# Kernel optimization log

Hardware: AMD Instinct MI355X
Metric: run time of the kernel (lower is better)

Reference implementation:

```python
import jax, jax.numpy as jnp
import numpy as np

EPS_IN = 1e-5   # InstanceNorm2d default eps
EPS_VAR = 1e-6  # clamp on attention variance

def instance_norm(x):
    # x: (b, c, h, w); affine=False, biased variance over spatial dims
    mean = jnp.mean(x, axis=(2, 3), keepdims=True)
    var = jnp.var(x, axis=(2, 3), keepdims=True)
    return (x - mean) * jax.lax.rsqrt(var + EPS_IN)

def setup_inputs() -> dict:
    key = jax.random.key(0)
    k1, k2, k3, k4 = jax.random.split(key, 4)
    shp = (4, 512, 64, 64)
    return {
        "c_x": jax.random.normal(k1, shp, dtype=jnp.float32),
        "s_x": jax.random.normal(k2, shp, dtype=jnp.float32),
        "c_1x": jax.random.normal(k3, shp, dtype=jnp.float32),
        "s_1x": jax.random.normal(k4, shp, dtype=jnp.float32),
    }

def reference(c_x, s_x, c_1x, s_1x):
    b, v_dim, h, w = c_x.shape
    hw = h * w
    # Q: (b, hw, qk), K: (b, qk, hw), V: (b, hw, v)
    Q = instance_norm(c_1x).reshape(b, -1, hw).transpose(0, 2, 1)
    K = instance_norm(s_1x).reshape(b, -1, s_1x.shape[2] * s_1x.shape[3])
    V = s_x.reshape(b, v_dim, -1).transpose(0, 2, 1)
    # attention over spatial tokens
    A = jax.nn.softmax(jnp.einsum('bqc,bck->bqk', Q, K), axis=-1)
    M = jnp.einsum('bqk,bkv->bqv', A, V)              # weighted mean
    Var = jnp.einsum('bqk,bkv->bqv', A, V * V) - M * M  # weighted variance
    S = jnp.sqrt(jnp.clip(Var, EPS_VAR, None))
    # back to (b, v, h, w)
    M = M.reshape(b, h, w, -1).transpose(0, 3, 1, 2)
    S = S.reshape(b, h, w, -1).transpose(0, 3, 1, 2)
    return S * instance_norm(c_x) + M
```

## Files before the change

### kernel.cpp

```cpp
#include <hip/hip_runtime.h>
#include <cmath>


#define B_  4
#define C_  512
#define HW_ 4096

typedef _Float16 f16;
typedef _Float16 f16x8 __attribute__((ext_vector_type(8)));
typedef float    f32x4 __attribute__((ext_vector_type(4)));

__device__ __forceinline__ f32x4 mfma16(f16x8 a, f16x8 b, f32x4 c) {
  return __builtin_amdgcn_mfma_f32_16x16x32_f16(a, b, c, 0, 0, 0);
}
__device__ __forceinline__ void g2l16(const f16* g, f16* l) {
  __builtin_amdgcn_global_load_lds(
      (const __attribute__((address_space(1))) void*)g,
      (__attribute__((address_space(3))) void*)l, 16, 0, 0);
}

__global__ __launch_bounds__(256) void k_stats(
    const float* __restrict__ cx, const float* __restrict__ c1,
    const float* __restrict__ s1,
    float2* __restrict__ cxs, float2* __restrict__ c1s, float2* __restrict__ s1s) {
  int c = blockIdx.x, b = blockIdx.y, t = blockIdx.z;
  const float* src = (t == 0 ? cx : (t == 1 ? c1 : s1)) + (size_t)(b * C_ + c) * HW_;
  float s = 0.f, q = 0.f;
  const float4* src4 = (const float4*)src;
  for (int i = threadIdx.x; i < HW_ / 4; i += 256) {
    float4 v = src4[i];
    s += v.x + v.y + v.z + v.w;
    q += v.x * v.x + v.y * v.y + v.z * v.z + v.w * v.w;
  }
#pragma unroll
  for (int off = 1; off < 64; off <<= 1) {
    s += __shfl_xor(s, off);
    q += __shfl_xor(q, off);
  }
  __shared__ float ss[4], sq[4];
  int wv = threadIdx.x >> 6;
  if ((threadIdx.x & 63) == 0) { ss[wv] = s; sq[wv] = q; }
  __syncthreads();
  if (threadIdx.x == 0) {
    float S = ss[0] + ss[1] + ss[2] + ss[3];
    float Q = sq[0] + sq[1] + sq[2] + sq[3];
    float mean = S * (1.f / HW_);
    float var = Q * (1.f / HW_) - mean * mean;
    float2 r;
    r.x = mean;
    r.y = rsqrtf(var + 1e-5f);
    (t == 0 ? cxs : (t == 1 ? c1s : s1s))[b * C_ + c] = r;
  }
}

__global__ __launch_bounds__(256) void k_prept(
    const float* __restrict__ src, const float2* __restrict__ st,
    f16* __restrict__ dst) {
  int pb = blockIdx.x * 64, cb = blockIdx.y * 64, b = blockIdx.z;
  __shared__ float t[64][65];
  int tj = threadIdx.x & 63, tr = threadIdx.x >> 6;
#pragma unroll 4
  for (int p = 0; p < 16; ++p) {
    int cl = p * 4 + tr;
    float2 mr = st[b * C_ + cb + cl];
    float v = src[(size_t)(b * C_ + cb + cl) * HW_ + pb + tj];
    t[cl][tj] = (v - mr.x) * mr.y;
  }
  __syncthreads();
#pragma unroll 4
  for (int p = 0; p < 16; ++p) {
    int pr = p * 4 + tr;
    dst[(size_t)(b * HW_ + pb + pr) * C_ + cb + tj] = (f16)t[tj][pr];
  }
}

__global__ __launch_bounds__(256) void k_prepv(const float* __restrict__ src,
                                               f16* __restrict__ dst) {
  int gid = blockIdx.x * 256 + threadIdx.x;
  const float4* s = (const float4*)src + (size_t)gid * 2;
  float4 v0 = s[0], v1 = s[1];
  f16x8 v = {(f16)v0.x, (f16)v0.y, (f16)v0.z, (f16)v0.w,
             (f16)v1.x, (f16)v1.y, (f16)v1.z, (f16)v1.w};
  *(f16x8*)(dst + (size_t)gid * 8) = v;
}

__global__ __launch_bounds__(512, 2) void k_qk(
    const f16* __restrict__ Qt, const f16* __restrict__ Kt,
    f16* __restrict__ E, float2* __restrict__ mlpart,
    int qspan, int qt256, int npair) {
  int id = blockIdx.x, pair, kt;
  if ((npair & 7) == 0) {
    int xcd = id & 7, j = id >> 3, qrs = npair >> 3;
    pair = xcd * qrs + (j % qrs);
    kt = j / qrs;
  } else {
    pair = id >> 4;
    kt = id & 15;
  }
  int bz = pair / qt256, qt = pair - bz * qt256;

  const f16* Aq = Qt + ((size_t)(bz * qspan + qt * 256)) * C_;
  const f16* Bk = Kt + (size_t)bz * HW_ * C_ + (size_t)kt * 256 * C_;
  f16* Eb = E + ((size_t)(bz * qspan + qt * 256)) * HW_ + kt * 256;
  float2* mlb = mlpart + ((size_t)(bz * qspan + qt * 256)) * 16 + kt;

  __shared__ __align__(16) union ShQK {
    f16 ring[3 * 16384];
    f16 ebuf[64 * 272];
  } sh;
  __shared__ float sred[2][256];

  int t = threadIdx.x, wave = t >> 6, lane = t & 63, lq = lane & 15, quad = lane >> 4;
  int wy = wave >> 1, wx = wave & 1;
  int srow = t >> 2, scol = (t & 3) * 8;

  int aoff = (wy * 64 + lq) * 32 + quad * 8;
  int boff = (wx * 128 + lq) * 32 + quad * 8;

  f32x4 acc[4][8];
#pragma unroll
  for (int mt = 0; mt < 4; ++mt)
#pragma unroll
    for (int nt = 0; nt < 8; ++nt) acc[mt][nt] = (f32x4){0, 0, 0, 0};

#pragma unroll
  for (int s0 = 0; s0 < 2; ++s0) {
    int off = s0 * 16384;
    g2l16(Aq + (size_t)srow * C_ + s0 * 32 + scol, sh.ring + off + t * 8);
    g2l16(Aq + (size_t)(128 + srow) * C_ + s0 * 32 + scol, sh.ring + off + 4096 + t * 8);
    g2l16(Bk + (size_t)srow * C_ + s0 * 32 + scol, sh.ring + off + 8192 + t * 8);
    g2l16(Bk + (size_t)(128 + srow) * C_ + s0 * 32 + scol, sh.ring + off + 12288 + t * 8);
  }
  asm volatile("s_waitcnt vmcnt(4)" ::: "memory");
  __builtin_amdgcn_s_barrier();

  int cur = 0, pn = 2;
  for (int s = 0; s < 16; ++s) {
    const f16* As_s = sh.ring + cur * 16384;
    const f16* Bs_s = As_s + 8192;
    int pnOff = pn * 16384;
    bool st = s < 14;

    f16x8 af[4], bf[8];
#pragma unroll
    for (int mt = 0; mt < 4; ++mt)
      af[mt] = *(const f16x8*)(As_s + aoff + mt * 512);
#pragma unroll
    for (int nt = 0; nt < 8; ++nt)
      bf[nt] = *(const f16x8*)(Bs_s + boff + nt * 512);

    if (st) {
      int c2 = (s + 2) * 32;
      g2l16(Aq + (size_t)srow * C_ + c2 + scol, sh.ring + pnOff + t * 8);
      g2l16(Aq + (size_t)(128 + srow) * C_ + c2 + scol, sh.ring + pnOff + 4096 + t * 8);
      g2l16(Bk + (size_t)srow * C_ + c2 + scol, sh.ring + pnOff + 8192 + t * 8);
      g2l16(Bk + (size_t)(128 + srow) * C_ + c2 + scol, sh.ring + pnOff + 12288 + t * 8);
    }
    asm volatile("s_waitcnt lgkmcnt(0)" ::: "memory");
    __builtin_amdgcn_sched_barrier(0);
    __builtin_amdgcn_s_setprio(1);
#pragma unroll
    for (int mt = 0; mt < 4; ++mt)
#pragma unroll
      for (int nt = 0; nt < 8; ++nt)
        acc[mt][nt] = mfma16(af[mt], bf[nt], acc[mt][nt]);
    __builtin_amdgcn_s_setprio(0);
    if (st) { asm volatile("s_waitcnt vmcnt(4)" ::: "memory"); }
    else    { asm volatile("s_waitcnt vmcnt(0)" ::: "memory"); }
    __builtin_amdgcn_s_barrier();

    cur = (cur == 2) ? 0 : cur + 1;
    pn = (pn == 2) ? 0 : pn + 1;
  }

#pragma unroll
  for (int mt = 0; mt < 4; ++mt)
#pragma unroll
    for (int r = 0; r < 4; ++r) {
      float v = -1e30f;
#pragma unroll
      for (int nt = 0; nt < 8; ++nt) v = fmaxf(v, acc[mt][nt][r]);
#pragma unroll
      for (int msk = 1; msk < 16; msk <<= 1) v = fmaxf(v, __shfl_xor(v, msk));
      if (lq == 0) sred[wx][wy * 64 + mt * 16 + quad * 4 + r] = v;
    }
  __syncthreads();
  float mrow[4][4];
#pragma unroll
  for (int mt = 0; mt < 4; ++mt)
#pragma unroll
    for (int r = 0; r < 4; ++r) {
      int rr = wy * 64 + mt * 16 + quad * 4 + r;
      mrow[mt][r] = fmaxf(sred[0][rr], sred[1][rr]);
    }

  float rsum[4][4];
#pragma unroll
  for (int mt = 0; mt < 4; ++mt)
#pragma unroll
    for (int r = 0; r < 4; ++r) rsum[mt][r] = 0.f;

#pragma unroll
  for (int mt = 0; mt < 4; ++mt) {
    __syncthreads();
#pragma unroll
    for (int nt = 0; nt < 8; ++nt) {
      f32x4 v = acc[mt][nt];
      int cs = ((wx * 16 + nt * 2 + (lq >> 3)) ^ (quad << 1)) * 8 + (lq & 7);
#pragma unroll
      for (int r = 0; r < 4; ++r) {
        float e = __expf(v[r] - mrow[mt][r]);
        rsum[mt][r] += e;
        sh.ebuf[(wy * 16 + quad * 4 + r) * 272 + cs] = (f16)e;
      }
    }
    __syncthreads();
#pragma unroll
    for (int i = 0; i < 4; ++i) {
      int idx = i * 512 + t;
      int rl = idx >> 5, ck = idx & 31;
      int cr = (ck ^ (((rl >> 2) & 3) << 1)) * 8;
      f16x8 v8 = *(const f16x8*)(sh.ebuf + rl * 272 + cr);
      int grow = (rl >> 4) * 64 + mt * 16 + (rl & 15);
      *(f16x8*)(Eb + (size_t)grow * HW_ + ck * 8) = v8;
    }
  }

#pragma unroll
  for (int mt = 0; mt < 4; ++mt)
#pragma unroll
    for (int r = 0; r < 4; ++r) {
      float v = rsum[mt][r];
#pragma unroll
      for (int msk = 1; msk < 16; msk <<= 1) v += __shfl_xor(v, msk);
      if (lq == 0) sred[wx][wy * 64 + mt * 16 + quad * 4 + r] = v;
    }
  __syncthreads();
  if (wx == 0 && lq == 0) {
#pragma unroll
    for (int mt = 0; mt < 4; ++mt)
#pragma unroll
      for (int r = 0; r < 4; ++r) {
        int rr = wy * 64 + mt * 16 + quad * 4 + r;
        mlb[(size_t)rr * 16] = make_float2(mrow[mt][r], sred[0][rr] + sred[1][rr]);
      }
  }
}

__global__ __launch_bounds__(256) void k_red(const float2* __restrict__ mlpart,
                                             float* __restrict__ alpha) {
  int row = blockIdx.x * 256 + threadIdx.x;
  const float2* p = mlpart + (size_t)row * 16;
  float2 loc[16];
  float m = -1e30f;
#pragma unroll
  for (int i = 0; i < 16; ++i) {
    loc[i] = p[i];
    m = fmaxf(m, loc[i].x);
  }
  float l = 0.f;
#pragma unroll
  for (int i = 0; i < 16; ++i) l += loc[i].y * __expf(loc[i].x - m);
  float invl = 1.f / l;
#pragma unroll
  for (int i = 0; i < 16; ++i)
    alpha[(size_t)row * 16 + i] = __expf(loc[i].x - m) * invl;
}

#define PV_STAGE_A(i)                                                         \
  g2l16(Ap + (size_t)((i)*64 + srow) * HW_ + s2 * 64 + scol,                  \
        sm + pnOff + (i)*4096 + t * 8)
#define PV_STAGE_B(i)                                                         \
  g2l16(Bv + (size_t)((i)*64 + srow) * HW_ + s2 * 64 + scol,                  \
        sm + pnOff + 16384 + (i)*4096 + t * 8)

#define PV_PHASE(CX, STAGE_STMT, POST_STMT)                                   \
  {                                                                           \
    f16x8 af0 = *(const f16x8*)(As_s + aoff + 0 * 1024 + (CX));               \
    f16x8 af1 = *(const f16x8*)(As_s + aoff + 1 * 1024 + (CX));               \
    f16x8 af2 = *(const f16x8*)(As_s + aoff + 2 * 1024 + (CX));               \
    f16x8 af3 = *(const f16x8*)(As_s + aoff + 3 * 1024 + (CX));               \
    f16x8 bf0 = *(const f16x8*)(Bs_s + boff + 0 * 1024 + (CX));               \
    f16x8 bf1 = *(const f16x8*)(Bs_s + boff + 1 * 1024 + (CX));               \
    f16x8 bf2 = *(const f16x8*)(Bs_s + boff + 2 * 1024 + (CX));               \
    f16x8 bf3 = *(const f16x8*)(Bs_s + boff + 3 * 1024 + (CX));               \
    STAGE_STMT;                                                               \
    asm volatile("s_waitcnt lgkmcnt(0)" ::: "memory");                        \
    __builtin_amdgcn_sched_barrier(0);                                        \
    __builtin_amdgcn_s_setprio(1);                                            \
    af0 *= aal[0]; af1 *= aal[1]; af2 *= aal[2]; af3 *= aal[3];               \
    f16x8 q0 = bf0 * bf0, q1 = bf1 * bf1, q2 = bf2 * bf2, q3 = bf3 * bf3;     \
    accM [0][0] = mfma16(af0, bf0, accM [0][0]);                              \
    accM2[0][0] = mfma16(af0, q0,  accM2[0][0]);                              \
    accM [0][1] = mfma16(af0, bf1, accM [0][1]);                              \
    accM2[0][1] = mfma16(af0, q1,  accM2[0][1]);                              \
    accM [0][2] = mfma16(af0, bf2, accM [0][2]);                              \
    accM2[0][2] = mfma16(af0, q2,  accM2[0][2]);                              \
    accM [0][3] = mfma16(af0, bf3, accM [0][3]);                              \
    accM2[0][3] = mfma16(af0, q3,  accM2[0][3]);                              \
    accM [1][0] = mfma16(af1, bf0, accM [1][0]);                              \
    accM2[1][0] = mfma16(af1, q0,  accM2[1][0]);                              \
    accM [1][1] = mfma16(af1, bf1, accM [1][1]);                              \
    accM2[1][1] = mfma16(af1, q1,  accM2[1][1]);                              \
    accM [1][2] = mfma16(af1, bf2, accM [1][2]);                              \
    accM2[1][2] = mfma16(af1, q2,  accM2[1][2]);                              \
    accM [1][3] = mfma16(af1, bf3, accM [1][3]);                              \
    accM2[1][3] = mfma16(af1, q3,  accM2[1][3]);                              \
    accM [2][0] = mfma16(af2, bf0, accM [2][0]);                              \
    accM2[2][0] = mfma16(af2, q0,  accM2[2][0]);                              \
    accM [2][1] = mfma16(af2, bf1, accM [2][1]);                              \
    accM2[2][1] = mfma16(af2, q1,  accM2[2][1]);                              \
    accM [2][2] = mfma16(af2, bf2, accM [2][2]);                              \
    accM2[2][2] = mfma16(af2, q2,  accM2[2][2]);                              \
    accM [2][3] = mfma16(af2, bf3, accM [2][3]);                              \
    accM2[2][3] = mfma16(af2, q3,  accM2[2][3]);                              \
    accM [3][0] = mfma16(af3, bf0, accM [3][0]);                              \
    accM2[3][0] = mfma16(af3, q0,  accM2[3][0]);                              \
    accM [3][1] = mfma16(af3, bf1, accM [3][1]);                              \
    accM2[3][1] = mfma16(af3, q1,  accM2[3][1]);                              \
    accM [3][2] = mfma16(af3, bf2, accM [3][2]);                              \
    accM2[3][2] = mfma16(af3, q2,  accM2[3][2]);                              \
    accM [3][3] = mfma16(af3, bf3, accM [3][3]);                              \
    accM2[3][3] = mfma16(af3, q3,  accM2[3][3]);                              \
    __builtin_amdgcn_s_setprio(0);                                            \
    POST_STMT;                                                                \
  }

__global__ __launch_bounds__(512, 2) void k_pv(
    const f16* __restrict__ P, const float* __restrict__ alphaG,
    const f16* __restrict__ V, const float* __restrict__ cx,
    const float2* __restrict__ cxs, float* __restrict__ out,
    int qspan, int qbase, int qt256) {
  int npairs = (int)gridDim.x >> 2;
  int id = blockIdx.x, pair, ct;
  if ((npairs & 7) == 0) {
    int x = id & 7, j = id >> 3, ppx = npairs >> 3;
    pair = x * ppx + (j >> 2);
    ct = j & 3;
  } else {
    pair = id >> 2;
    ct = id & 3;
  }
  int bz = pair / qt256, qt = pair - bz * qt256;

  const f16* Ap = P + ((size_t)(bz * qspan + qt * 256)) * HW_;
  const f16* Bv = V + ((size_t)(bz * C_ + ct * 128)) * HW_;

  __shared__ __align__(16) f16 sm[3 * 24576 + 256 * 17];
  f16* Alh = sm + 3 * 24576;

  int t = threadIdx.x, wave = t >> 6, lane = t & 63, lq = lane & 15, quad = lane >> 4;
  int wy = wave >> 1, wx = wave & 1;

  {
    const float* ag = alphaG + ((size_t)(bz * qspan + qt * 256)) * 16;
#pragma unroll
    for (int i = 0; i < 8; ++i) {
      int e = i * 512 + t;
      Alh[(e >> 4) * 17 + (e & 15)] = (f16)ag[e];
    }
  }

  int srow = t >> 3;
  int scol = ((t & 7) ^ (srow & 7)) * 8;

  int aoff = (wy * 64 + lq) * 64;
  int boff = (wx * 64 + lq) * 64;
  int cx0 = (quad * 8) ^ ((lq & 7) << 3);
  int cx1 = (32 + quad * 8) ^ ((lq & 7) << 3);

  f32x4 accM[4][4], accM2[4][4];
#pragma unroll
  for (int mt = 0; mt < 4; ++mt)
#pragma unroll
    for (int nt = 0; nt < 4; ++nt) {
      accM[mt][nt] = (f32x4){0, 0, 0, 0};
      accM2[mt][nt] = (f32x4){0, 0, 0, 0};
    }

#pragma unroll
  for (int s0 = 0; s0 < 2; ++s0) {
    int off = s0 * 24576;
#pragma unroll
    for (int i = 0; i < 4; ++i)
      g2l16(Ap + (size_t)(i * 64 + srow) * HW_ + s0 * 64 + scol,
            sm + off + i * 4096 + t * 8);
#pragma unroll
    for (int i = 0; i < 2; ++i)
      g2l16(Bv + (size_t)(i * 64 + srow) * HW_ + s0 * 64 + scol,
            sm + off + 16384 + i * 4096 + t * 8);
  }
  asm volatile("s_waitcnt lgkmcnt(0)" ::: "memory");
  asm volatile("s_waitcnt vmcnt(6)" ::: "memory");
  __builtin_amdgcn_s_barrier();

  int ph = 0, pn = 2;
  for (int s = 0; s < 64; ++s) {
    const f16* As_s = sm + ph * 24576;
    const f16* Bs_s = As_s + 16384;
    int pnOff = pn * 24576;
    int s2 = s + 2;
    bool st = s < 62;
    int ktl = s >> 2;
    f16 aal[4];
    aal[0] = Alh[(wy * 64 + lq +  0) * 17 + ktl];
    aal[1] = Alh[(wy * 64 + lq + 16) * 17 + ktl];
    aal[2] = Alh[(wy * 64 + lq + 32) * 17 + ktl];
    aal[3] = Alh[(wy * 64 + lq + 48) * 17 + ktl];

    PV_PHASE(cx0,
             if (st) { PV_STAGE_A(0); PV_STAGE_A(1); PV_STAGE_A(2); }, )
    PV_PHASE(cx1,
             if (st) { PV_STAGE_A(3); PV_STAGE_B(0); PV_STAGE_B(1); },
             if (st) { asm volatile("s_waitcnt vmcnt(6)" ::: "memory"); }
             else    { asm volatile("s_waitcnt vmcnt(0)" ::: "memory"); })
    __builtin_amdgcn_s_barrier();

    ph = (ph == 2) ? 0 : ph + 1;
    pn = (pn == 2) ? 0 : pn + 1;
  }

  int chbase = ct * 128 + wx * 64;
#pragma unroll
  for (int mt = 0; mt < 4; ++mt) {
    int q0 = qbase + qt * 256 + wy * 64 + mt * 16 + quad * 4;
#pragma unroll
    for (int nt = 0; nt < 4; ++nt) {
      int c = chbase + nt * 16 + lq;
      float2 stc = cxs[bz * C_ + c];
      size_t base = ((size_t)bz * C_ + c) * HW_ + q0;
      float4 cv = *(const float4*)(cx + base);
      f32x4 m1 = accM[mt][nt], m2 = accM2[mt][nt];
      float4 o;
      o.x = sqrtf(fmaxf(m2[0] - m1[0] * m1[0], 1e-6f)) * ((cv.x - stc.x) * stc.y) + m1[0];
      o.y = sqrtf(fmaxf(m2[1] - m1[1] * m1[1], 1e-6f)) * ((cv.y - stc.x) * stc.y) + m1[1];
      o.z = sqrtf(fmaxf(m2[2] - m1[2] * m1[2], 1e-6f)) * ((cv.z - stc.x) * stc.y) + m1[2];
      o.w = sqrtf(fmaxf(m2[3] - m1[3] * m1[3], 1e-6f)) * ((cv.w - stc.x) * stc.y) + m1[3];
      *(float4*)(out + base) = o;
    }
  }
}

extern "C" void kernel_launch(void* const* d_in, const int* in_sizes, int n_in,
                              void* d_out, int out_size, void* d_ws,
                              size_t ws_size, hipStream_t stream) {
  const float* c_x = (const float*)d_in[0];
  const float* s_x = (const float*)d_in[1];
  const float* c1x = (const float*)d_in[2];
  const float* s1x = (const float*)d_in[3];
  float* out = (float*)d_out;

  char* ws = (char*)d_ws;
  size_t o = 0;
  f16* Qt = (f16*)(ws + o);  o += (size_t)B_ * HW_ * C_ * 2;
  f16* Kt = (f16*)(ws + o);  o += (size_t)B_ * HW_ * C_ * 2;
  f16* Vh = (f16*)(ws + o);  o += (size_t)B_ * HW_ * C_ * 2;
  float2* cxs = (float2*)(ws + o); o += B_ * C_ * sizeof(float2);
  float2* c1s = (float2*)(ws + o); o += B_ * C_ * sizeof(float2);
  float2* s1s = (float2*)(ws + o); o += B_ * C_ * sizeof(float2);
  size_t fixed = (o + 255) & ~(size_t)255;

  const size_t per_row = (size_t)HW_ * 2 + 16 * 8 + 16 * 4;
  struct Cfg { int nb, qs; };
  const Cfg cfgs[5] = {{4, 4096}, {1, 4096}, {1, 2048}, {1, 1024}, {1, 512}};
  Cfg cfg = cfgs[4];
  for (int i = 0; i < 5; ++i) {
    size_t rows = (size_t)cfgs[i].nb * cfgs[i].qs;
    if (fixed + rows * per_row <= ws_size) { cfg = cfgs[i]; break; }
  }
  const int nb = cfg.nb, qspan = cfg.qs, qt256 = qspan / 256;
  const int npair256 = nb * qt256;
  const size_t rows = (size_t)nb * qspan;
  f16* E = (f16*)(ws + fixed);
  float2* mlpart = (float2*)(ws + fixed + rows * HW_ * 2);
  float* alpha = (float*)(ws + fixed + rows * HW_ * 2 + rows * 16 * 8);

  k_stats<<<dim3(C_, B_, 3), 256, 0, stream>>>(c_x, c1x, s1x, cxs, c1s, s1s);
  k_prept<<<dim3(HW_ / 64, C_ / 64, B_), 256, 0, stream>>>(c1x, c1s, Qt);
  k_prept<<<dim3(HW_ / 64, C_ / 64, B_), 256, 0, stream>>>(s1x, s1s, Kt);
  k_prepv<<<dim3(B_ * C_ * HW_ / 8 / 256), 256, 0, stream>>>(s_x, Vh);

  for (int b0 = 0; b0 < B_; b0 += nb) {
    for (int qb = 0; qb < HW_; qb += qspan) {
      const f16* Qtp = Qt + ((size_t)b0 * HW_ + qb) * C_;
      const f16* Ktp = Kt + (size_t)b0 * HW_ * C_;
      const f16* Vp = Vh + (size_t)b0 * C_ * HW_;
      const float* cxp = c_x + (size_t)b0 * C_ * HW_;
      const float2* cxsp = cxs + b0 * C_;
      float* outp = out + (size_t)b0 * C_ * HW_;

      k_qk<<<dim3((unsigned)(npair256 * 16)), 512, 0, stream>>>(
          Qtp, Ktp, E, mlpart, qspan, qt256, npair256);
      k_red<<<dim3((unsigned)(rows / 256)), 256, 0, stream>>>(mlpart, alpha);
      k_pv<<<dim3((unsigned)(npair256 * 4)), 512, 0, stream>>>(
          E, alpha, Vp, cxp, cxsp, outp, qspan, qb, qt256);
    }
  }
}
```

Measured before the change: 386.4 us.

## Use double-buffered 64-wide K tiles with XOR-swizzled LDS in QK GEMM

Replaces the 3-stage ring of 32-wide K slices with a 2-stage double buffer of 64-wide slices, halving the number of main-loop barriers. It adds an XOR swizzle on the LDS layout to avoid bank conflicts on the wider rows. Global-to-LDS loads for the next tile are split across the two MFMA half-steps. Prefetch depth drops from two stages to one, and each iteration waits for vmcnt(0), so global load latency may be less well hidden.

```diff
diff --git a/kernel.cpp b/kernel.cpp
--- a/kernel.cpp
+++ b/kernel.cpp
@@ -105,17 +105,21 @@
   float2* mlb = mlpart + ((size_t)(bz * qspan + qt * 256)) * 16 + kt;
 
   __shared__ __align__(16) union ShQK {
-    f16 ring[3 * 16384];
+    f16 ring[2 * 32768];
     f16 ebuf[64 * 272];
   } sh;
   __shared__ float sred[2][256];
 
   int t = threadIdx.x, wave = t >> 6, lane = t & 63, lq = lane & 15, quad = lane >> 4;
   int wy = wave >> 1, wx = wave & 1;
-  int srow = t >> 2, scol = (t & 3) * 8;
-
-  int aoff = (wy * 64 + lq) * 32 + quad * 8;
-  int boff = (wx * 128 + lq) * 32 + quad * 8;
+
+  int srow = t >> 3;
+  int scol = ((t & 7) ^ (srow & 7)) * 8;
+
+  int aoff = (wy * 64 + lq) * 64;
+  int boff = 16384 + (wx * 128 + lq) * 64;
+  int cx0 = (quad * 8) ^ ((lq & 7) << 3);
+  int cx1 = (32 + quad * 8) ^ ((lq & 7) << 3);
 
   f32x4 acc[4][8];
 #pragma unroll
@@ -124,37 +128,33 @@
     for (int nt = 0; nt < 8; ++nt) acc[mt][nt] = (f32x4){0, 0, 0, 0};
 
 #pragma unroll
-  for (int s0 = 0; s0 < 2; ++s0) {
-    int off = s0 * 16384;
-    g2l16(Aq + (size_t)srow * C_ + s0 * 32 + scol, sh.ring + off + t * 8);
-    g2l16(Aq + (size_t)(128 + srow) * C_ + s0 * 32 + scol, sh.ring + off + 4096 + t * 8);
-    g2l16(Bk + (size_t)srow * C_ + s0 * 32 + scol, sh.ring + off + 8192 + t * 8);
-    g2l16(Bk + (size_t)(128 + srow) * C_ + s0 * 32 + scol, sh.ring + off + 12288 + t * 8);
-  }
-  asm volatile("s_waitcnt vmcnt(4)" ::: "memory");
+  for (int i = 0; i < 4; ++i)
+    g2l16(Aq + (size_t)(i * 64 + srow) * C_ + scol, sh.ring + i * 4096 + t * 8);
+#pragma unroll
+  for (int i = 0; i < 4; ++i)
+    g2l16(Bk + (size_t)(i * 64 + srow) * C_ + scol, sh.ring + 16384 + i * 4096 + t * 8);
+  asm volatile("s_waitcnt vmcnt(0)" ::: "memory");
   __builtin_amdgcn_s_barrier();
 
-  int cur = 0, pn = 2;
-  for (int s = 0; s < 16; ++s) {
-    const f16* As_s = sh.ring + cur * 16384;
-    const f16* Bs_s = As_s + 8192;
-    int pnOff = pn * 16384;
-    bool st = s < 14;
+  int cur = 0;
+  for (int s = 0; s < 8; ++s) {
+    const f16* base = sh.ring + cur * 32768;
+    int nxOff = (cur ^ 1) * 32768;
+    bool st = s < 7;
+    int c1g = (s + 1) * 64;
 
     f16x8 af[4], bf[8];
 #pragma unroll
     for (int mt = 0; mt < 4; ++mt)
-      af[mt] = *(const f16x8*)(As_s + aoff + mt * 512);
+      af[mt] = *(const f16x8*)(base + aoff + mt * 1024 + cx0);
 #pragma unroll
     for (int nt = 0; nt < 8; ++nt)
-      bf[nt] = *(const f16x8*)(Bs_s + boff + nt * 512);
-
+      bf[nt] = *(const f16x8*)(base + boff + nt * 1024 + cx0);
     if (st) {
-      int c2 = (s + 2) * 32;
-      g2l16(Aq + (size_t)srow * C_ + c2 + scol, sh.ring + pnOff + t * 8);
-      g2l16(Aq + (size_t)(128 + srow) * C_ + c2 + scol, sh.ring + pnOff + 4096 + t * 8);
-      g2l16(Bk + (size_t)srow * C_ + c2 + scol, sh.ring + pnOff + 8192 + t * 8);
-      g2l16(Bk + (size_t)(128 + srow) * C_ + c2 + scol, sh.ring + pnOff + 12288 + t * 8);
+#pragma unroll
+      for (int i = 0; i < 4; ++i)
+        g2l16(Aq + (size_t)(i * 64 + srow) * C_ + c1g + scol,
+              sh.ring + nxOff + i * 4096 + t * 8);
     }
     asm volatile("s_waitcnt lgkmcnt(0)" ::: "memory");
     __builtin_amdgcn_sched_barrier(0);
@@ -165,12 +165,32 @@
       for (int nt = 0; nt < 8; ++nt)
         acc[mt][nt] = mfma16(af[mt], bf[nt], acc[mt][nt]);
     __builtin_amdgcn_s_setprio(0);
-    if (st) { asm volatile("s_waitcnt vmcnt(4)" ::: "memory"); }
-    else    { asm volatile("s_waitcnt vmcnt(0)" ::: "memory"); }
+
+#pragma unroll
+    for (int mt = 0; mt < 4; ++mt)
+      af[mt] = *(const f16x8*)(base + aoff + mt * 1024 + cx1);
+#pragma unroll
+    for (int nt = 0; nt < 8; ++nt)
+      bf[nt] = *(const f16x8*)(base + boff + nt * 1024 + cx1);
+    if (st) {
+#pragma unroll
+      for (int i = 0; i < 4; ++i)
+        g2l16(Bk + (size_t)(i * 64 + srow) * C_ + c1g + scol,
+              sh.ring + nxOff + 16384 + i * 4096 + t * 8);
+    }
+    asm volatile("s_waitcnt lgkmcnt(0)" ::: "memory");
+    __builtin_amdgcn_sched_barrier(0);
+    __builtin_amdgcn_s_setprio(1);
+#pragma unroll
+    for (int mt = 0; mt < 4; ++mt)
+#pragma unroll
+      for (int nt = 0; nt < 8; ++nt)
+        acc[mt][nt] = mfma16(af[mt], bf[nt], acc[mt][nt]);
+    __builtin_amdgcn_s_setprio(0);
+
+    asm volatile("s_waitcnt vmcnt(0)" ::: "memory");
     __builtin_amdgcn_s_barrier();
-
-    cur = (cur == 2) ? 0 : cur + 1;
-    pn = (pn == 2) ? 0 : pn + 1;
+    cur ^= 1;
   }
 
 #pragma unroll
```

Measured after the change: 390.6 us. About the same (+1.1%).
